# Kernel optimization log

Hardware: AMD Instinct MI355X
Metric: run time of the kernel (lower is better)

Reference implementation:

```python
import jax, jax.numpy as jnp
import numpy as np

B, T = 128, 100
DZ, DA, DU, K, DOBS, H = 64, 32, 8, 8, 16, 128
JITTER = 1e-4  # _safe_cholesky: sym + jitter*I, then first try adds 1.0*jitter*I again


def setup_inputs() -> dict:
    key = jax.random.key(0)
    ks = jax.random.split(key, 10)
    eye_z = jnp.eye(DZ, dtype=jnp.float32)
    # stable-ish per-component transition matrices
    A_mats = 0.9 * eye_z[None] + 0.05 * jax.random.normal(ks[0], (K, DZ, DZ), jnp.float32)
    B_mats = 0.1 * jax.random.normal(ks[1], (K, DZ, DU), jnp.float32)
    C_mats = 0.3 * jax.random.normal(ks[2], (K, DA, DZ), jnp.float32)
    a_seq = jax.random.normal(ks[3], (B, T, DA), jnp.float32)
    h_obs = jax.random.normal(ks[4], (B, DOBS), jnp.float32)
    u_seq = jax.random.normal(ks[5], (B, T, DU), jnp.float32)
    mask = jnp.ones((B, T), jnp.float32)
    a_0 = jnp.zeros((1, DA), jnp.float32)          # nn.Parameter a_0
    P_0 = 10.0 * eye_z                              # 10 * eye(dim_z)
    Q = 0.05 * eye_z                                # Q_std * eye(dim_z)
    R = 0.05 * jnp.eye(DA, dtype=jnp.float32)       # R_std * eye(dim_a)
    din = DA + DOBS + DU
    s = 1.0 / float(np.sqrt(H))
    W_ih = s * jax.random.normal(ks[6], (3 * H, din), jnp.float32)
    W_hh = s * jax.random.normal(ks[7], (3 * H, H), jnp.float32)
    b_ih = jnp.zeros((3 * H,), jnp.float32)
    b_hh = jnp.zeros((3 * H,), jnp.float32)
    W_out = s * jax.random.normal(ks[8], (K, H), jnp.float32)
    b_out = jnp.zeros((K,), jnp.float32)
    return dict(a_seq=a_seq, h_obs=h_obs, u_seq=u_seq, mask=mask,
                A_mats=A_mats, B_mats=B_mats, C_mats=C_mats,
                a_0=a_0, P_0=P_0, Q=Q, R=R,
                W_ih=W_ih, W_hh=W_hh, b_ih=b_ih, b_hh=b_hh,
                W_out=W_out, b_out=b_out, epoch=100)


def _sym(M):
    return 0.5 * (M + jnp.swapaxes(M, -1, -2))


def _gru_alpha(x, h, W_ih, W_hh, b_ih, b_hh, W_out, b_out):
    # GRU-cell alpha_net: mixture weights over K components
    gi = x @ W_ih.T + b_ih
    gh = h @ W_hh.T + b_hh
    ir, iz, inn = jnp.split(gi, 3, axis=-1)
    hr, hz, hn = jnp.split(gh, 3, axis=-1)
    r = jax.nn.sigmoid(ir + hr)
    zg = jax.nn.sigmoid(iz + hz)
    n = jnp.tanh(inn + r * hn)
    h_new = (1.0 - zg) * n + zg * h
    alpha = jax.nn.softmax(h_new @ W_out.T + b_out, axis=-1)
    return alpha, h_new


def _kalman_forward(a_seq, h_obs, u_seq, mask, A_mats, B_mats, C_mats,
                    a_0, P_0, Q, R, W_ih, W_hh, b_ih, b_hh, W_out, b_out):
    Bsz = a_seq.shape[0]
    I = jnp.eye(DZ, dtype=a_seq.dtype)

    def mix(alpha):
        A = jnp.einsum('bk,kij->bij', alpha, A_mats)
        Bc = jnp.einsum('bk,kij->bij', alpha, B_mats)
        C = jnp.einsum('bk,kij->bij', alpha, C_mats)
        return A, Bc, C

    def alpha_net(a, u, h):
        x = jnp.concatenate([a, h_obs, u], axis=-1)
        return _gru_alpha(x, h, W_ih, W_hh, b_ih, b_hh, W_out, b_out)

    gru_h = jnp.zeros((Bsz, H), a_seq.dtype)
    a_prev = jnp.broadcast_to(a_0, (Bsz, DA))
    alpha0, gru_h = alpha_net(a_prev, u_seq[:, 0], gru_h)
    A_k0, B_k0, C_k0 = mix(alpha0)

    z0 = jnp.zeros((Bsz, DZ), a_seq.dtype)
    P0 = jnp.broadcast_to(P_0, (Bsz, DZ, DZ))

    def step(carry, inp):
        z_prev, P, h, A_k, B_k, C_k = carry
        a_k, u_k, m_k = inp  # [B,da], [B,du], [B]
        mk = m_k[:, None]
        # predict with matrices chosen at previous step
        z = jnp.einsum('bij,bj->bi', A_k, z_prev) + jnp.einsum('bij,bj->bi', B_k, u_k)
        a_hat = jnp.einsum('bij,bj->bi', C_k, z)
        r_k = a_k - a_hat
        CP = jnp.einsum('bij,bjk->bik', C_k, P)                      # C P
        S = jnp.einsum('bik,bjk->bij', CP, C_k) + R                   # C P C^T + R
        # K = solve(S^T, C P^T)^T  (i.e. K = P C^T S^{-1})
        CPt = jnp.einsum('bij,bkj->bik', C_k, P)
        Kg = jnp.swapaxes(jnp.linalg.solve(jnp.swapaxes(S, -1, -2), CPt), -1, -2)
        Kg = Kg * m_k[:, None, None]
        IKC = I - jnp.einsum('bij,bjk->bik', Kg, C_k)
        # Joseph form update
        P_filt = (jnp.einsum('bij,bjk,blk->bil', IKC, P, IKC)
                  + jnp.einsum('bij,jk,blk->bil', Kg, R, Kg))
        P_filt = _sym(P_filt)
        z_mean = z + jnp.einsum('bij,bj->bi', Kg, r_k)
        L = jnp.linalg.cholesky(_sym(P_filt) + 2.0 * JITTER * I)      # safe cholesky
        z_filt = z_mean                                               # dist.mean
        a_filt = jnp.einsum('bij,bj->bi', C_k, z_filt)
        a_k_hat = mk * a_k + (1.0 - mk) * a_filt
        C_old = C_k
        alpha, h = alpha_net(a_k_hat, u_k, h)
        A_n, B_n, C_n = mix(alpha)
        z_pred = (jnp.einsum('bij,bj->bi', A_n, z_filt)
                  + jnp.einsum('bij,bj->bi', B_n, u_k))
        a_pred = jnp.einsum('bij,bj->bi', C_n, z_pred)
        P_pred = _sym(jnp.einsum('bij,bjk,blk->bil', A_n, P_filt, A_n) + Q)
        carry = (z_filt, P_pred, h, A_n, B_n, C_n)
        out = (z_filt, P_filt, z_pred, P_pred, alpha, a_filt, a_pred,
               S, z_mean, L, A_n, B_n, C_old)
        return carry, out

    xs = (jnp.swapaxes(a_seq, 0, 1), jnp.swapaxes(u_seq, 0, 1), jnp.swapaxes(mask, 0, 1))
    _, outs = jax.lax.scan(step, (z0, P0, gru_h, A_k0, B_k0, C_k0), xs)
    # scan outputs are [T, B, ...] -> [B, T, ...]
    (z_filt, P_filt, z_pred, P_pred, alpha_seq, a_filt, a_pred,
     S_pred, z_means, z_scale_tril, A_seq, B_seq, C_seq) = jax.tree.map(
        lambda x: jnp.swapaxes(x, 0, 1), outs)
    return (z_filt, P_filt, z_pred, a_filt, a_pred, P_pred, alpha_seq,
            A_seq, B_seq, C_seq, z_means, z_scale_tril, S_pred)


def reference(a_seq, h_obs, u_seq, mask, A_mats, B_mats, C_mats,
              a_0, P_0, Q, R, W_ih, W_hh, b_ih, b_hh, W_out, b_out, epoch):
    # epoch >= warmup/burn-in thresholds (all 0), so no detach branches apply
    return _kalman_forward(a_seq, h_obs, u_seq, mask, A_mats, B_mats, C_mats,
                           a_0, P_0, Q, R, W_ih, W_hh, b_ih, b_hh, W_out, b_out)
```

## Files before the change

kernel.cpp:

```cpp
#include <hip/hip_runtime.h>

typedef float f4 __attribute__((ext_vector_type(4)));

#define NT 256
#define BB 128
#define BT 100
#define DZc 64
#define DAc 32
#define DUc 8
#define KMIX 8
#define DOBSc 16
#define HG 128
#define DINc 56

#define O_ZFILT   0LL
#define O_PFILT   819200LL
#define O_ZPRED   53248000LL
#define O_AFILT   54067200LL
#define O_APRED   54476800LL
#define O_PPRED   54886400LL
#define O_ALPHA   107315200LL
#define O_ASEQ    107417600LL
#define O_BSEQ    159846400LL
#define O_CSEQ    166400000LL
#define O_ZMEAN   192614400LL
#define O_LTRIL   193433600LL
#define O_SPRED   245862400LL

__device__ __forceinline__ float dot4(f4 a, f4 b) {
    return a[0]*b[0] + a[1]*b[1] + a[2]*b[2] + a[3]*b[3];
}

struct SMem {
    float P[DZc][68];
    float A[DZc][68];
    float AT[DZc][68];
    float Wk[DZc][68];
    float Qm[DZc][68];
    float C[DAc][68];
    float CP[DAc][68];
    float Xm[DAc][68];
    float S[DAc][33];
    float Rm[DAc][33];
    float dinv[DAc];
    float Bm[DZc][8];
    float z[DZc], zp[DZc], zn[DZc];
    float h[HG], hn[HG];
    float gh[3*HG], gi[3*HG];
    float x[64];
    float ak[DAc], rvec[DAc];
    float u[8];
    float lg[8];
    float mk;
};

template<bool EMIT>
__device__ __forceinline__ void mix_apply(SMem& s, int tid, size_t bt, const float* al8,
    const float* __restrict__ A_mats, const float* __restrict__ B_mats,
    const float* __restrict__ C_mats, float* __restrict__ out)
{
    const f4* A4 = (const f4*)A_mats;
    const f4* B4 = (const f4*)B_mats;
    const f4* C4 = (const f4*)C_mats;
    #pragma unroll 2
    for (int e = 0; e < 4; ++e) {
        int i4 = tid + e*256;
        f4 acc = {0.f,0.f,0.f,0.f};
        #pragma unroll
        for (int k = 0; k < 8; ++k) acc += al8[k] * A4[k*1024 + i4];
        int row = i4 >> 4, cb = (i4 & 15) * 4;
        *(f4*)&s.A[row][cb] = acc;
        s.AT[cb][row] = acc[0]; s.AT[cb+1][row] = acc[1];
        s.AT[cb+2][row] = acc[2]; s.AT[cb+3][row] = acc[3];
        if (EMIT) *(f4*)&out[O_ASEQ + bt*4096 + (size_t)i4*4] = acc;
    }
    if (tid < 128) {
        int i4 = tid;
        f4 acc = {0.f,0.f,0.f,0.f};
        #pragma unroll
        for (int k = 0; k < 8; ++k) acc += al8[k] * B4[k*128 + i4];
        *(f4*)&s.Bm[i4>>1][(i4&1)*4] = acc;
        if (EMIT) *(f4*)&out[O_BSEQ + bt*512 + (size_t)i4*4] = acc;
    }
    #pragma unroll 1
    for (int e = 0; e < 2; ++e) {
        int i4 = tid + e*256;
        f4 acc = {0.f,0.f,0.f,0.f};
        #pragma unroll
        for (int k = 0; k < 8; ++k) acc += al8[k] * C4[k*512 + i4];
        *(f4*)&s.C[i4>>4][(i4&15)*4] = acc;
    }
}

__global__ void __launch_bounds__(NT, 1)
kalman_seq(const float* __restrict__ a_seq, const float* __restrict__ h_obs,
           const float* __restrict__ u_seq, const float* __restrict__ mask,
           const float* __restrict__ A_mats, const float* __restrict__ B_mats,
           const float* __restrict__ C_mats, const float* __restrict__ a_0,
           const float* __restrict__ P_0, const float* __restrict__ Q,
           const float* __restrict__ R, const float* __restrict__ W_ih,
           const float* __restrict__ W_hh, const float* __restrict__ b_ih,
           const float* __restrict__ b_hh, const float* __restrict__ W_out,
           const float* __restrict__ b_out, float* __restrict__ out)
{
    __shared__ SMem s;
    const int b = blockIdx.x;
    const int tid = threadIdx.x;
    const int r4 = (tid >> 4) << 2;
    const int c4 = (tid & 15) << 2;

    for (int idx = tid; idx < DZc*DZc; idx += NT) {
        s.P[idx >> 6][idx & 63]  = P_0[idx];
        s.Qm[idx >> 6][idx & 63] = Q[idx];
    }
    for (int idx = tid; idx < DAc*DAc; idx += NT) s.Rm[idx >> 5][idx & 31] = R[idx];
    if (tid < HG) s.h[tid] = 0.f;
    if (tid < DZc) s.z[tid] = 0.f;
    if (tid < DAc)                 s.x[tid] = a_0[tid];
    else if (tid < DAc + DOBSc)    s.x[tid] = h_obs[b*DOBSc + (tid - DAc)];
    else if (tid < DINc)           s.x[tid] = u_seq[(size_t)b*BT*DUc + (tid - DAc - DOBSc)];
    __syncthreads();

    for (int g = tid; g < 3*HG; g += NT) {
        const float* wi = W_ih + (size_t)g * DINc;
        f4 ai = {0.f,0.f,0.f,0.f};
        #pragma unroll 7
        for (int q = 0; q < 14; ++q) ai += *(const f4*)(wi + q*4) * *(const f4*)&s.x[q*4];
        s.gi[g] = ai[0]+ai[1]+ai[2]+ai[3] + b_ih[g];
        s.gh[g] = b_hh[g];
    }
    __syncthreads();
    if (tid < HG) {
        float r  = 1.f / (1.f + expf(-(s.gi[tid] + s.gh[tid])));
        float zg = 1.f / (1.f + expf(-(s.gi[HG+tid] + s.gh[HG+tid])));
        float n  = tanhf(s.gi[2*HG+tid] + r * s.gh[2*HG+tid]);
        s.h[tid] = (1.f - zg) * n;
    }
    __syncthreads();
    if (tid < KMIX) {
        const float* wo = W_out + tid * HG;
        f4 acc = {0.f,0.f,0.f,0.f};
        #pragma unroll 8
        for (int q = 0; q < 32; ++q) acc += *(const f4*)(wo + q*4) * *(const f4*)&s.h[q*4];
        s.lg[tid] = acc[0]+acc[1]+acc[2]+acc[3] + b_out[tid];
    }
    __syncthreads();
    {
        float lg[8];
        #pragma unroll
        for (int k = 0; k < 8; ++k) lg[k] = s.lg[k];
        float mx = lg[0];
        #pragma unroll
        for (int k = 1; k < 8; ++k) mx = fmaxf(mx, lg[k]);
        float al[8]; float sum = 0.f;
        #pragma unroll
        for (int k = 0; k < 8; ++k) { al[k] = expf(lg[k] - mx); sum += al[k]; }
        float rs = 1.f / sum;
        #pragma unroll
        for (int k = 0; k < 8; ++k) al[k] *= rs;
        mix_apply<false>(s, tid, 0, al, A_mats, B_mats, C_mats, out);
    }
    __syncthreads();

    for (int t = 0; t < BT; ++t) {
        const size_t bt = (size_t)b * BT + t;

        if (tid < 64) {
            float acc = 0.f;
            #pragma unroll 8
            for (int k = 0; k < DZc; ++k) acc += s.AT[k][tid] * s.z[k];
            const float* up = u_seq + bt*DUc;
            #pragma unroll
            for (int q = 0; q < DUc; ++q) acc += s.Bm[tid][q] * up[q];
            s.zp[tid] = acc;
        } else if (tid < 96) {
            float av = a_seq[bt*DAc + (tid-64)];
            s.ak[tid-64] = av;
            s.x[tid-64] = av;
        } else if (tid < 104) {
            float uv = u_seq[bt*DUc + (tid-96)];
            s.u[tid-96] = uv; s.x[48 + (tid-96)] = uv;
        } else if (tid == 104) {
            s.mk = mask[bt];
        }
        __syncthreads();
        const float mkv = s.mk;
        const bool mk1 = (mkv == 1.0f);

        {
            const int r = tid >> 3;
            const int c8 = (tid & 7) * 8;
            f4 acc0 = {0.f,0.f,0.f,0.f}, acc1 = {0.f,0.f,0.f,0.f};
            #pragma unroll 4
            for (int k4 = 0; k4 < 16; ++k4) {
                f4 cr = *(const f4*)&s.C[r][k4*4];
                #pragma unroll
                for (int kk = 0; kk < 4; ++kk) {
                    float cv = cr[kk];
                    acc0 += cv * *(const f4*)&s.P[k4*4+kk][c8];
                    acc1 += cv * *(const f4*)&s.P[k4*4+kk][c8+4];
                }
            }
            *(f4*)&s.CP[r][c8]   = acc0;
            *(f4*)&s.CP[r][c8+4] = acc1;
        }
        if (tid < DAc) {
            float acc = 0.f;
            #pragma unroll 4
            for (int k4 = 0; k4 < 16; ++k4)
                acc += dot4(*(const f4*)&s.C[tid][k4*4], *(const f4*)&s.zp[k4*4]);
            s.rvec[tid] = s.ak[tid] - acc;
        }
        __syncthreads();

        {
            const int r = tid >> 3;
            const int cb = (tid & 7) * 4;
            f4 acc = {0.f,0.f,0.f,0.f};
            #pragma unroll 4
            for (int k4 = 0; k4 < 16; ++k4) {
                f4 a = *(const f4*)&s.CP[r][k4*4];
                #pragma unroll
                for (int j = 0; j < 4; ++j)
                    acc[j] += dot4(a, *(const f4*)&s.C[cb+j][k4*4]);
            }
            f4 rm = {s.Rm[r][cb], s.Rm[r][cb+1], s.Rm[r][cb+2], s.Rm[r][cb+3]};
            f4 v = acc + rm;
            s.S[r][cb] = v[0]; s.S[r][cb+1] = v[1]; s.S[r][cb+2] = v[2]; s.S[r][cb+3] = v[3];
            *(f4*)&out[O_SPRED + bt*1024 + (size_t)r*32 + cb] = v;
        }
        __syncthreads();

        if (tid < 64) {
            const int lane = tid;
            const int l = lane & 31, par = lane >> 5;
            for (int k = 0; k < 31; ++k) {
                __threadfence_block();
                float dv = 1.0f / s.S[k][k];
                if (lane == k) s.dinv[k] = dv;
                if (l > k) {
                    float f = s.S[l][k] * dv;
                    for (int j = k + 1 + par; j <= l; j += 2)
                        s.S[l][j] -= f * s.S[j][k];
                }
            }
            __threadfence_block();
            if (lane == 31) s.dinv[31] = 1.0f / s.S[31][31];
            __threadfence_block();
            float v[32];
            #pragma unroll
            for (int r = 0; r < 32; ++r) v[r] = s.CP[r][lane];
            #pragma unroll
            for (int r = 0; r < 32; ++r) {
                float acc = v[r];
                #pragma unroll
                for (int k = 0; k < r; ++k) acc -= s.S[r][k] * v[k];
                v[r] = s.dinv[r] * acc;
            }
            #pragma unroll
            for (int r = 30; r >= 0; --r) {
                float acc = 0.f;
                #pragma unroll
                for (int k = r+1; k < 32; ++k) acc += s.S[k][r] * v[k];
                v[r] -= s.dinv[r] * acc;
            }
            float accz = 0.f;
            #pragma unroll
            for (int r = 0; r < 32; ++r) {
                s.Xm[r][lane] = v[r];
                accz += v[r] * s.rvec[r];
            }
            s.zn[lane] = s.zp[lane] + mkv * accz;
            __threadfence_block();
            if (lane < DAc) {
                float acc = 0.f;
                #pragma unroll 4
                for (int k4 = 0; k4 < 16; ++k4)
                    acc += dot4(*(const f4*)&s.C[lane][k4*4], *(const f4*)&s.zn[k4*4]);
                out[O_AFILT + bt*DAc + lane] = acc;
                if (!mk1) s.x[lane] = mkv * s.ak[lane] + (1.f - mkv) * acc;
            }
        } else if (tid < 192) {
            const int idx = tid - 64;
            const float* wir = W_ih + (size_t)idx * DINc;
            const float* wiz = W_ih + (size_t)(HG + idx) * DINc;
            const float* win = W_ih + (size_t)(2*HG + idx) * DINc;
            const float* whr = W_hh + (size_t)idx * HG;
            const float* whz = W_hh + (size_t)(HG + idx) * HG;
            const float* whn = W_hh + (size_t)(2*HG + idx) * HG;
            f4 air = {0.f,0.f,0.f,0.f}, aiz = {0.f,0.f,0.f,0.f}, ain = {0.f,0.f,0.f,0.f};
            #pragma unroll 7
            for (int q = 0; q < 14; ++q) {
                f4 xv = *(const f4*)&s.x[q*4];
                air += *(const f4*)(wir + q*4) * xv;
                aiz += *(const f4*)(wiz + q*4) * xv;
                ain += *(const f4*)(win + q*4) * xv;
            }
            f4 ahr = {0.f,0.f,0.f,0.f}, ahz = {0.f,0.f,0.f,0.f}, ahn = {0.f,0.f,0.f,0.f};
            #pragma unroll 8
            for (int q = 0; q < 32; ++q) {
                f4 hv = *(const f4*)&s.h[q*4];
                ahr += *(const f4*)(whr + q*4) * hv;
                ahz += *(const f4*)(whz + q*4) * hv;
                ahn += *(const f4*)(whn + q*4) * hv;
            }
            float gir = air[0]+air[1]+air[2]+air[3] + b_ih[idx];
            float giz = aiz[0]+aiz[1]+aiz[2]+aiz[3] + b_ih[HG + idx];
            float gin = ain[0]+ain[1]+ain[2]+ain[3] + b_ih[2*HG + idx];
            float ghr = ahr[0]+ahr[1]+ahr[2]+ahr[3] + b_hh[idx];
            float ghz = ahz[0]+ahz[1]+ahz[2]+ahz[3] + b_hh[HG + idx];
            float ghn = ahn[0]+ahn[1]+ahn[2]+ahn[3] + b_hh[2*HG + idx];
            float r  = 1.f / (1.f + expf(-(gir + ghr)));
            float zg = 1.f / (1.f + expf(-(giz + ghz)));
            float n  = tanhf(gin + r * ghn);
            s.hn[idx] = (1.f - zg) * n + zg * s.h[idx];
        } else {
            const int l = tid - 192;
            #pragma unroll 2
            for (int e = 0; e < 8; ++e) {
                int i4 = l + e*64;
                *(f4*)&out[O_CSEQ + bt*2048 + (size_t)i4*4] = *(const f4*)&s.C[i4>>4][(i4&15)*4];
            }
        }
        __syncthreads();

        {
            const float coef = (mkv*mkv - 2.f*mkv) * 0.5f;
            f4 acc0 = {0.f,0.f,0.f,0.f}, acc1 = {0.f,0.f,0.f,0.f};
            f4 acc2 = {0.f,0.f,0.f,0.f}, acc3 = {0.f,0.f,0.f,0.f};
            #pragma unroll 4
            for (int l = 0; l < DAc; ++l) {
                f4 cpc = *(const f4*)&s.CP[l][c4];
                f4 xc  = *(const f4*)&s.Xm[l][c4];
                f4 cpr = *(const f4*)&s.CP[l][r4];
                f4 xr  = *(const f4*)&s.Xm[l][r4];
                acc0 += xr[0]*cpc + cpr[0]*xc;
                acc1 += xr[1]*cpc + cpr[1]*xc;
                acc2 += xr[2]*cpc + cpr[2]*xc;
                acc3 += xr[3]*cpc + cpr[3]*xc;
            }
            #pragma unroll
            for (int i = 0; i < 4; ++i) {
                const int row = r4 + i;
                f4 g = (i==0) ? acc0 : (i==1) ? acc1 : (i==2) ? acc2 : acc3;
                f4 p = *(const f4*)&s.P[row][c4];
                f4 v = p + coef * g;
                *(f4*)&s.P[row][c4] = v;
                *(f4*)&out[O_PFILT + bt*4096 + (size_t)row*64 + c4] = v;
            }
        }
        if (tid < DZc) {
            float v = s.zn[tid];
            out[O_ZFILT + bt*DZc + tid] = v;
            out[O_ZMEAN + bt*DZc + tid] = v;
            s.z[tid] = v;
        }

        if (!mk1) {
            __syncthreads();
            for (int g = tid; g < 3*HG; g += NT) {
                const float* wi = W_ih + (size_t)g * DINc;
                const float* wh = W_hh + (size_t)g * HG;
                f4 ai = {0.f,0.f,0.f,0.f}, ah = {0.f,0.f,0.f,0.f};
                #pragma unroll 7
                for (int q = 0; q < 14; ++q) ai += *(const f4*)(wi + q*4) * *(const f4*)&s.x[q*4];
                #pragma unroll 8
                for (int q = 0; q < 32; ++q) ah += *(const f4*)(wh + q*4) * *(const f4*)&s.h[q*4];
                s.gi[g] = ai[0]+ai[1]+ai[2]+ai[3] + b_ih[g];
                s.gh[g] = ah[0]+ah[1]+ah[2]+ah[3] + b_hh[g];
            }
            __syncthreads();
            if (tid < HG) {
                float gi0 = s.gi[tid], gi1 = s.gi[HG+tid], gi2 = s.gi[2*HG+tid];
                float gh0 = s.gh[tid], gh1 = s.gh[HG+tid], gh2 = s.gh[2*HG+tid];
                float hold = s.h[tid];
                float r  = 1.f / (1.f + expf(-(gi0 + gh0)));
                float zg = 1.f / (1.f + expf(-(gi1 + gh1)));
                float n  = tanhf(gi2 + r * gh2);
                s.hn[tid] = (1.f - zg) * n + zg * hold;
            }
            __syncthreads();
        }

        {
            const int lane = tid & 63;
            const int g = lane >> 3;
            const int cb = (lane & 7) * 16;
            f4 a4 = {0.f,0.f,0.f,0.f};
            #pragma unroll
            for (int q = 0; q < 4; ++q)
                a4 += *(const f4*)(W_out + (size_t)g*HG + cb + q*4) * *(const f4*)&s.hn[cb + q*4];
            float acc = a4[0]+a4[1]+a4[2]+a4[3];
            acc += __shfl_xor(acc, 1); acc += __shfl_xor(acc, 2); acc += __shfl_xor(acc, 4);
            float lg[8];
            #pragma unroll
            for (int k = 0; k < 8; ++k) lg[k] = __shfl(acc, k*8) + b_out[k];
            float mx = lg[0];
            #pragma unroll
            for (int k = 1; k < 8; ++k) mx = fmaxf(mx, lg[k]);
            float al[8]; float sum = 0.f;
            #pragma unroll
            for (int k = 0; k < 8; ++k) { al[k] = expf(lg[k] - mx); sum += al[k]; }
            float rs = 1.f / sum;
            #pragma unroll
            for (int k = 0; k < 8; ++k) al[k] *= rs;
            if (tid < 8) out[O_ALPHA + bt*8 + tid] = al[tid];
            mix_apply<true>(s, tid, bt, al, A_mats, B_mats, C_mats, out);
        }
        if (tid < HG) s.h[tid] = s.hn[tid];
        __syncthreads();

        if (tid < 64) {
            float acc = 0.f;
            #pragma unroll 8
            for (int k = 0; k < DZc; ++k) acc += s.AT[k][tid] * s.z[k];
            acc += dot4(*(const f4*)&s.Bm[tid][0], *(const f4*)&s.u[0]);
            acc += dot4(*(const f4*)&s.Bm[tid][4], *(const f4*)&s.u[4]);
            s.zp[tid] = acc;
            out[O_ZPRED + bt*DZc + tid] = acc;
        }
        {
            f4 acc[4] = {{0.f,0.f,0.f,0.f},{0.f,0.f,0.f,0.f},{0.f,0.f,0.f,0.f},{0.f,0.f,0.f,0.f}};
            #pragma unroll 2
            for (int k4 = 0; k4 < 16; ++k4) {
                f4 ar0 = *(const f4*)&s.A[r4+0][k4*4];
                f4 ar1 = *(const f4*)&s.A[r4+1][k4*4];
                f4 ar2 = *(const f4*)&s.A[r4+2][k4*4];
                f4 ar3 = *(const f4*)&s.A[r4+3][k4*4];
                #pragma unroll
                for (int kk = 0; kk < 4; ++kk) {
                    f4 bv = *(const f4*)&s.P[k4*4+kk][c4];
                    acc[0] += ar0[kk] * bv; acc[1] += ar1[kk] * bv;
                    acc[2] += ar2[kk] * bv; acc[3] += ar3[kk] * bv;
                }
            }
            #pragma unroll
            for (int i = 0; i < 4; ++i)
                *(f4*)&s.Wk[r4+i][c4] = acc[i];
        }
        __syncthreads();

        {
            f4 acc[4] = {{0.f,0.f,0.f,0.f},{0.f,0.f,0.f,0.f},{0.f,0.f,0.f,0.f},{0.f,0.f,0.f,0.f}};
            #pragma unroll 2
            for (int k4 = 0; k4 < 16; ++k4) {
                f4 w0 = *(const f4*)&s.Wk[r4+0][k4*4];
                f4 w1 = *(const f4*)&s.Wk[r4+1][k4*4];
                f4 w2 = *(const f4*)&s.Wk[r4+2][k4*4];
                f4 w3 = *(const f4*)&s.Wk[r4+3][k4*4];
                #pragma unroll
                for (int kk = 0; kk < 4; ++kk) {
                    f4 av = *(const f4*)&s.AT[k4*4+kk][c4];
                    acc[0] += w0[kk] * av; acc[1] += w1[kk] * av;
                    acc[2] += w2[kk] * av; acc[3] += w3[kk] * av;
                }
            }
            #pragma unroll
            for (int i = 0; i < 4; ++i) {
                const int row = r4 + i;
                f4 q = *(const f4*)&s.Qm[row][c4];
                f4 v = acc[i] + q;
                *(f4*)&s.P[row][c4] = v;
                *(f4*)&out[O_PPRED + bt*4096 + (size_t)row*64 + c4] = v;
            }
        }
        if (tid < DAc) {
            float acc = 0.f;
            #pragma unroll 4
            for (int k4 = 0; k4 < 16; ++k4)
                acc += dot4(*(const f4*)&s.C[tid][k4*4], *(const f4*)&s.zp[k4*4]);
            out[O_APRED + bt*DAc + tid] = acc;
        }
        __syncthreads();
    }
}

__global__ void __launch_bounds__(64)
chol_batch(float* __restrict__ out)
{
    __shared__ float M[DZc][65];
    __shared__ float sd[DZc];
    const size_t bt = blockIdx.x;
    const int lane = threadIdx.x;
    const float* src = out + O_PFILT + bt*4096;
    #pragma unroll 4
    for (int e = 0; e < 16; ++e) {
        int i4 = lane + e*64;
        f4 v = *(const f4*)(src + (size_t)i4*4);
        int row = i4 >> 4, cb = (i4 & 15) * 4;
        M[row][cb] = v[0]; M[row][cb+1] = v[1]; M[row][cb+2] = v[2]; M[row][cb+3] = v[3];
    }
    __syncthreads();
    M[lane][lane] += 2.0e-4f;
    __syncthreads();
    for (int k = 0; k < DZc; ++k) {
        __threadfence_block();
        float mkk = M[k][k];
        if (lane == k) sd[k] = sqrtf(mkk);
        if (lane > k) {
            float f = M[lane][k] / mkk;
            for (int j = k + 1; j <= lane; ++j)
                M[lane][j] -= f * M[j][k];
        }
    }
    __threadfence_block();
    for (int k = 0; k < lane; ++k) M[lane][k] /= sd[k];
    M[lane][lane] = sd[lane];
    for (int k = lane + 1; k < DZc; ++k) M[lane][k] = 0.f;
    __syncthreads();
    float* dst = out + O_LTRIL + bt*4096;
    #pragma unroll 4
    for (int e = 0; e < 16; ++e) {
        int i4 = lane + e*64;
        int row = i4 >> 4, cb = (i4 & 15) * 4;
        f4 v = {M[row][cb], M[row][cb+1], M[row][cb+2], M[row][cb+3]};
        *(f4*)(dst + (size_t)i4*4) = v;
    }
}

extern "C" void kernel_launch(void* const* d_in, const int* in_sizes, int n_in,
                              void* d_out, int out_size, void* d_ws, size_t ws_size,
                              hipStream_t stream) {
    const float* a_seq  = (const float*)d_in[0];
    const float* h_obs  = (const float*)d_in[1];
    const float* u_seq  = (const float*)d_in[2];
    const float* mask   = (const float*)d_in[3];
    const float* A_mats = (const float*)d_in[4];
    const float* B_mats = (const float*)d_in[5];
    const float* C_mats = (const float*)d_in[6];
    const float* a_0    = (const float*)d_in[7];
    const float* P_0    = (const float*)d_in[8];
    const float* Q      = (const float*)d_in[9];
    const float* R      = (const float*)d_in[10];
    const float* W_ih   = (const float*)d_in[11];
    const float* W_hh   = (const float*)d_in[12];
    const float* b_ih   = (const float*)d_in[13];
    const float* b_hh   = (const float*)d_in[14];
    const float* W_out  = (const float*)d_in[15];
    const float* b_out  = (const float*)d_in[16];
    float* out = (float*)d_out;

    kalman_seq<<<dim3(BB), dim3(NT), 0, stream>>>(a_seq, h_obs, u_seq, mask,
        A_mats, B_mats, C_mats, a_0, P_0, Q, R, W_ih, W_hh, b_ih, b_hh, W_out, b_out, out);
    chol_batch<<<dim3(BB*BT), dim3(64), 0, stream>>>(out);
}
```

Measured before the change: 7.302 ms.

## Register-resident Cholesky rows with broadcast column buffer; pad AT and reduce GRU unroll

The 32x32 Cholesky factorization now keeps each lane's row of S in registers. Each step broadcasts column k through a small shared buffer, replacing the strided shared-memory updates spread over two lane halves. The AT array is padded to 72 columns to change its bank mapping, and the GRU dot-product unroll factors are reduced to lower register pressure. The fully unrolled 32-step loop raises register use in the Cholesky section, and the upper half of the wavefront does redundant work.

```diff
diff --git a/kernel.cpp b/kernel.cpp
--- a/kernel.cpp
+++ b/kernel.cpp
@@ -34,7 +34,7 @@
 struct SMem {
     float P[DZc][68];
     float A[DZc][68];
-    float AT[DZc][68];
+    float AT[DZc][72];
     float Wk[DZc][68];
     float Qm[DZc][68];
     float C[DAc][68];
@@ -43,6 +43,7 @@
     float S[DAc][33];
     float Rm[DAc][33];
     float dinv[DAc];
+    float col[64];
     float Bm[DZc][8];
     float z[DZc], zp[DZc], zn[DZc];
     float h[HG], hn[HG];
@@ -233,19 +234,35 @@
 
         if (tid < 64) {
             const int lane = tid;
-            const int l = lane & 31, par = lane >> 5;
-            for (int k = 0; k < 31; ++k) {
+            const int l = lane & 31;
+            float row[32];
+            #pragma unroll
+            for (int j = 0; j < 32; ++j) row[j] = s.S[l][j];
+            #pragma unroll
+            for (int k = 0; k < 32; ++k) {
+                if (lane < 32) s.col[lane] = row[k];
                 __threadfence_block();
-                float dv = 1.0f / s.S[k][k];
+                float cb[32];
+                #pragma unroll
+                for (int jv = 0; jv < 8; ++jv) {
+                    if (jv*4 + 3 >= k) {
+                        f4 cv = *(const f4*)&s.col[jv*4];
+                        cb[jv*4] = cv[0]; cb[jv*4+1] = cv[1];
+                        cb[jv*4+2] = cv[2]; cb[jv*4+3] = cv[3];
+                    }
+                }
+                float dv = 1.0f / cb[k];
                 if (lane == k) s.dinv[k] = dv;
-                if (l > k) {
-                    float f = s.S[l][k] * dv;
-                    for (int j = k + 1 + par; j <= l; j += 2)
-                        s.S[l][j] -= f * s.S[j][k];
-                }
-            }
-            __threadfence_block();
-            if (lane == 31) s.dinv[31] = 1.0f / s.S[31][31];
+                float fm = (l > k) ? (row[k] * dv) : 0.f;
+                #pragma unroll
+                for (int j = k+1; j < 32; ++j)
+                    row[j] -= fm * cb[j];
+                __threadfence_block();
+            }
+            if (lane < 32) {
+                #pragma unroll
+                for (int j = 0; j < 32; ++j) s.S[l][j] = row[j];
+            }
             __threadfence_block();
             float v[32];
             #pragma unroll
@@ -289,7 +306,7 @@
             const float* whz = W_hh + (size_t)(HG + idx) * HG;
             const float* whn = W_hh + (size_t)(2*HG + idx) * HG;
             f4 air = {0.f,0.f,0.f,0.f}, aiz = {0.f,0.f,0.f,0.f}, ain = {0.f,0.f,0.f,0.f};
-            #pragma unroll 7
+            #pragma unroll 4
             for (int q = 0; q < 14; ++q) {
                 f4 xv = *(const f4*)&s.x[q*4];
                 air += *(const f4*)(wir + q*4) * xv;
@@ -297,7 +314,7 @@
                 ain += *(const f4*)(win + q*4) * xv;
             }
             f4 ahr = {0.f,0.f,0.f,0.f}, ahz = {0.f,0.f,0.f,0.f}, ahn = {0.f,0.f,0.f,0.f};
-            #pragma unroll 8
+            #pragma unroll 4
             for (int q = 0; q < 32; ++q) {
                 f4 hv = *(const f4*)&s.h[q*4];
                 ahr += *(const f4*)(whr + q*4) * hv;
```

Measured after the change: 6.496 ms. 1.12x faster.
